# Kernel optimization log

Hardware: AMD Instinct MI355X
Metric: run time of the kernel (lower is better)

The kernel has to match this reference:

```python
import jax, jax.numpy as jnp
import numpy as np

B, T, C = 2, 2048, 1024
H = 16
D = C // H  # head_size = 64
FF = 4 * C
EPS = 1e-5


def _layernorm(x, g, b):
    mu = jnp.mean(x, axis=-1, keepdims=True)
    var = jnp.var(x, axis=-1, keepdims=True)
    return (x - mu) * jax.lax.rsqrt(var + EPS) * g + b


def setup_inputs() -> dict:
    key = jax.random.key(0)
    ks = jax.random.split(key, 12)
    s_in = 1.0 / np.sqrt(C)
    s_ff = 1.0 / np.sqrt(FF)
    return {
        "x": jax.random.normal(ks[0], (B, T, C), jnp.float32),
        "Wq": jax.random.uniform(ks[1], (H, C, D), jnp.float32, -s_in, s_in),
        "Wk": jax.random.uniform(ks[2], (H, C, D), jnp.float32, -s_in, s_in),
        "Wv": jax.random.uniform(ks[3], (H, C, D), jnp.float32, -s_in, s_in),
        "Wo": jax.random.uniform(ks[4], (C, C), jnp.float32, -s_in, s_in),
        "bo": jax.random.uniform(ks[5], (C,), jnp.float32, -s_in, s_in),
        "W1": jax.random.uniform(ks[6], (C, FF), jnp.float32, -s_in, s_in),
        "b1": jax.random.uniform(ks[7], (FF,), jnp.float32, -s_in, s_in),
        "W2": jax.random.uniform(ks[8], (FF, C), jnp.float32, -s_ff, s_ff),
        "b2": jax.random.uniform(ks[9], (C,), jnp.float32, -s_ff, s_ff),
        "g1": jnp.ones((C,), jnp.float32),
        "be1": jnp.zeros((C,), jnp.float32),
        "g2": jnp.ones((C,), jnp.float32),
        "be2": jnp.zeros((C,), jnp.float32),
    }


def reference(x, Wq, Wk, Wv, Wo, bo, W1, b1, W2, b2, g1, be1, g2, be2):
    h = _layernorm(x, g1, be1)
    # per-head projections (no bias), vectorized over heads
    q = jnp.einsum("btc,hcd->bhtd", h, Wq)
    k = jnp.einsum("btc,hcd->bhtd", h, Wk)
    v = jnp.einsum("btc,hcd->bhtd", h, Wv)
    # NOTE: original scales by n_embd**-0.5 (C, not head_size) -- faithful
    scores = jnp.einsum("bhtd,bhsd->bhts", q, k) * (C ** -0.5)
    causal = jnp.tril(jnp.ones((T, T), bool))
    scores = jnp.where(causal, scores, -jnp.inf)
    att = jax.nn.softmax(scores, axis=-1)
    out = jnp.einsum("bhts,bhsd->bhtd", att, v)
    out = out.transpose(0, 2, 1, 3).reshape(B, T, C)  # concat heads
    x = out @ Wo + bo + x  # attn residual (dropout=0 -> identity)
    h2 = _layernorm(x, g2, be2)
    ff = jax.nn.relu(h2 @ W1 + b1) @ W2 + b2
    return x + ff
```

## Files before the change

kernel.cpp:

```cpp
#include <hip/hip_runtime.h>
#include <stdint.h>

typedef unsigned short ushort_t;
typedef __attribute__((ext_vector_type(8))) short bf16x8;
typedef __attribute__((ext_vector_type(4))) float f32x4;

__device__ __forceinline__ unsigned short f2b(float f) {
  unsigned u = __float_as_uint(f);
  u += 0x7fffu + ((u >> 16) & 1u);
  return (unsigned short)(u >> 16);
}

__device__ __forceinline__ void async16(const void* g, void* l) {
  __builtin_amdgcn_global_load_lds(
      (const __attribute__((address_space(1))) void*)g,
      (__attribute__((address_space(3))) void*)l, 16, 0, 0);
}

__global__ __launch_bounds__(256) void ln_kernel(
    const float* __restrict__ x, const float* __restrict__ g,
    const float* __restrict__ be, ushort_t* __restrict__ out) {
  const int C = 1024;
  int row = blockIdx.x;
  const float4* xr = (const float4*)(x + (size_t)row * C);
  int tid = threadIdx.x;
  float4 v = xr[tid];
  float s = v.x + v.y + v.z + v.w;
  float sq = v.x * v.x + v.y * v.y + v.z * v.z + v.w * v.w;
  #pragma unroll
  for (int off = 32; off > 0; off >>= 1) {
    s += __shfl_xor(s, off);
    sq += __shfl_xor(sq, off);
  }
  __shared__ float ss[4], ssq[4];
  int wv = tid >> 6;
  if ((tid & 63) == 0) { ss[wv] = s; ssq[wv] = sq; }
  __syncthreads();
  s = ss[0] + ss[1] + ss[2] + ss[3];
  sq = ssq[0] + ssq[1] + ssq[2] + ssq[3];
  float mu = s * (1.f / C);
  float var = sq * (1.f / C) - mu * mu;
  float rs = rsqrtf(var + 1e-5f);
  float4 gv = ((const float4*)g)[tid];
  float4 bv = ((const float4*)be)[tid];
  ushort4 o;
  o.x = f2b((v.x - mu) * rs * gv.x + bv.x);
  o.y = f2b((v.y - mu) * rs * gv.y + bv.y);
  o.z = f2b((v.z - mu) * rs * gv.z + bv.z);
  o.w = f2b((v.w - mu) * rs * gv.w + bv.w);
  ((ushort4*)(out + (size_t)row * C))[tid] = o;
}

__global__ __launch_bounds__(256) void reduce2_kernel(
    const float* __restrict__ p0, const float* __restrict__ p1,
    const float* __restrict__ bias, const float* __restrict__ resid,
    float* __restrict__ out) {
  int idx = blockIdx.x * 256 + threadIdx.x;
  float4 a = ((const float4*)p0)[idx];
  float4 b = ((const float4*)p1)[idx];
  float4 r = ((const float4*)resid)[idx];
  float4 bi = ((const float4*)bias)[idx & 255];
  float4 o;
  o.x = a.x + b.x + r.x + bi.x;
  o.y = a.y + b.y + r.y + bi.y;
  o.z = a.z + b.z + r.z + bi.z;
  o.w = a.w + b.w + r.w + bi.w;
  ((float4*)out)[idx] = o;
}

__global__ __launch_bounds__(256) void transpose_all_kernel(
    const float* __restrict__ Wq, const float* __restrict__ Wk,
    const float* __restrict__ Wv, const float* __restrict__ Wo,
    const float* __restrict__ W1, const float* __restrict__ W2,
    ushort_t* __restrict__ qkvt, ushort_t* __restrict__ wot,
    ushort_t* __restrict__ w1t, ushort_t* __restrict__ w2t) {
  int bid = blockIdx.x;
  const float* in;
  ushort_t* out;
  int R, Cin, bx, by;
  if (bid < 3072) {
    int z = bid >> 6, rem = bid & 63;
    bx = rem & 1; by = rem >> 1;
    int wsel = z >> 4, h = z & 15;
    in = (wsel == 0 ? Wq : wsel == 1 ? Wk : Wv) + (size_t)h * 1024 * 64;
    out = qkvt + (size_t)wsel * 1024 * 1024 + (size_t)h * 1024 * 64;
    R = 1024; Cin = 64;
  } else if (bid < 4096) {
    int rem = bid - 3072;
    bx = rem & 31; by = rem >> 5;
    in = Wo; out = wot; R = 1024; Cin = 1024;
  } else if (bid < 8192) {
    int rem = bid - 4096;
    bx = rem & 127; by = rem >> 7;
    in = W1; out = w1t; R = 1024; Cin = 4096;
  } else {
    int rem = bid - 8192;
    bx = rem & 31; by = rem >> 5;
    in = W2; out = w2t; R = 4096; Cin = 1024;
  }
  __shared__ float tile[32][33];
  int c0 = bx * 32, r0 = by * 32;
  int tx = threadIdx.x, ty = threadIdx.y;
  #pragma unroll
  for (int i = 0; i < 4; i++)
    tile[ty + 8 * i][tx] = in[(size_t)(r0 + ty + 8 * i) * Cin + c0 + tx];
  __syncthreads();
  #pragma unroll
  for (int i = 0; i < 4; i++)
    out[(size_t)(c0 + ty + 8 * i) * R + r0 + tx] = f2b(tile[tx][ty + 8 * i]);
}

__global__ __launch_bounds__(256) void transpose_v_kernel(
    const ushort_t* __restrict__ qkv, ushort_t* __restrict__ vt) {
  __shared__ ushort_t tile[32][33];
  int bh = blockIdx.z;
  int b = bh >> 4, h = bh & 15;
  int d0 = blockIdx.x * 32, t0 = blockIdx.y * 32;
  int tx = threadIdx.x, ty = threadIdx.y;
  #pragma unroll
  for (int i = 0; i < 4; i++)
    tile[ty + 8 * i][tx] =
        qkv[(size_t)(b * 2048 + t0 + ty + 8 * i) * 3072 + 2048 + h * 64 + d0 + tx];
  __syncthreads();
  #pragma unroll
  for (int i = 0; i < 4; i++)
    vt[(size_t)(bh * 64 + d0 + ty + 8 * i) * 2048 + t0 + tx] = tile[tx][ty + 8 * i];
}

template <int BN, int N, int K, int FLAGS, int SK>
__global__ __launch_bounds__(256, 3) void gemm_bt_kernel(
    const ushort_t* __restrict__ A, const ushort_t* __restrict__ Bt,
    const float* __restrict__ bias, const float* __restrict__ resid,
    void* __restrict__ outv, float* __restrict__ pp0, float* __restrict__ pp1) {
  constexpr int KS = K / SK;
  __shared__ ushort_t Als[2][128 * 32];
  __shared__ ushort_t Bls[2][128 * 32];
  int tid = threadIdx.x, w = tid >> 6, lane = tid & 63, quad = lane >> 4, l16 = lane & 15;
  int fid = blockIdx.x;
  int bn_low = (fid >> 3) & 7;
  int meta = (fid & 7) | ((fid >> 6) << 3);
  int bm = meta & 31;
  int high = meta >> 5;
  int bn, zz;
  if constexpr (SK > 1) { zz = high; bn = bn_low; }
  else { zz = 0; bn = bn_low + 8 * high; }
  int bn0 = bn * 128, bm0 = bm * 128;
  int koff = (SK > 1) ? zz * KS : 0;
  int wm = (w >> 1) * 64, wn = (w & 1) * 64;
  f32x4 acc[4][4];
  #pragma unroll
  for (int i = 0; i < 4; i++)
    #pragma unroll
    for (int j = 0; j < 4; j++) acc[i][j] = f32x4{0.f, 0.f, 0.f, 0.f};
  const ushort_t* Ag = A + (size_t)bm0 * K + koff;
  const ushort_t* Bg = Bt + (size_t)bn0 * K + koff;
  int lr = lane >> 2, lco = (lane & 3) * 8;
  auto stage = [&](int k0, int bi) {
    async16(Ag + (size_t)(w * 32 + lr) * K + k0 + lco, &Als[bi][w * 1024]);
    async16(Ag + (size_t)(w * 32 + 16 + lr) * K + k0 + lco, &Als[bi][w * 1024 + 512]);
    async16(Bg + (size_t)(w * 32 + lr) * K + k0 + lco, &Bls[bi][w * 1024]);
    async16(Bg + (size_t)(w * 32 + 16 + lr) * K + k0 + lco, &Bls[bi][w * 1024 + 512]);
  };
  stage(0, 0);
  int s = 0;
  for (int k0 = 0; k0 < KS; k0 += 32, s ^= 1) {
    __syncthreads();
    if (k0 + 32 < KS) stage(k0 + 32, s ^ 1);
    bf16x8 af[4], bf[4];
    #pragma unroll
    for (int i = 0; i < 4; i++)
      af[i] = *(const bf16x8*)&Als[s][(wm + i * 16 + l16) * 32 + quad * 8];
    #pragma unroll
    for (int j = 0; j < 4; j++)
      bf[j] = *(const bf16x8*)&Bls[s][(wn + j * 16 + l16) * 32 + quad * 8];
    #pragma unroll
    for (int i = 0; i < 4; i++)
      #pragma unroll
      for (int j = 0; j < 4; j++)
        acc[i][j] = __builtin_amdgcn_mfma_f32_16x16x32_bf16(af[i], bf[j], acc[i][j], 0, 0, 0);
  }
  float* pdst = nullptr;
  if constexpr (SK > 1) pdst = zz ? pp1 : pp0;
  #pragma unroll
  for (int i = 0; i < 4; i++)
    #pragma unroll
    for (int j = 0; j < 4; j++)
      #pragma unroll
      for (int r = 0; r < 4; r++) {
        int row = bm0 + wm + i * 16 + quad * 4 + r;
        int col = bn0 + wn + j * 16 + l16;
        float v = acc[i][j][r];
        if constexpr (SK > 1) {
          pdst[(size_t)row * N + col] = v;
        } else {
          if constexpr (FLAGS & 4) v += bias[col];
          if constexpr (FLAGS & 8) v += resid[(size_t)row * N + col];
          if constexpr (FLAGS & 1) v = fmaxf(v, 0.f);
          if constexpr ((FLAGS & 2) != 0)
            ((ushort_t*)outv)[(size_t)row * N + col] = f2b(v);
          else
            ((float*)outv)[(size_t)row * N + col] = v;
        }
      }
}

template <int N, int K, int FLAGS, int SK>
__global__ __launch_bounds__(256, 3) void gemm_bt64_kernel(
    const ushort_t* __restrict__ A, const ushort_t* __restrict__ Bt,
    const float* __restrict__ bias, const float* __restrict__ resid,
    void* __restrict__ outv, float* __restrict__ pp0, float* __restrict__ pp1) {
  constexpr int KS = K / SK;
  constexpr int NBM = 32;
  constexpr int NBN = N / 64;
  constexpr int NWG = NBM * NBN * SK;
  __shared__ ushort_t Als[2][128 * 32];
  __shared__ ushort_t Bls[2][64 * 32];
  int tid = threadIdx.x, w = tid >> 6, lane = tid & 63, quad = lane >> 4, l16 = lane & 15;
  int bid = blockIdx.x;
  int swz = (bid & 7) * (NWG / 8) + (bid >> 3);
  int z = 0;
  if constexpr (SK > 1) { z = swz / (NBM * NBN); swz -= z * (NBM * NBN); }
  int bm = swz / NBN, bn = swz - bm * NBN;
  int bm0 = bm * 128, bn0 = bn * 64;
  int koff = z * KS;
  int wm = (w >> 1) * 64, wn = (w & 1) * 32;
  f32x4 acc[4][2];
  #pragma unroll
  for (int i = 0; i < 4; i++)
    #pragma unroll
    for (int j = 0; j < 2; j++) acc[i][j] = f32x4{0.f, 0.f, 0.f, 0.f};
  const ushort_t* Ag = A + (size_t)bm0 * K + koff;
  const ushort_t* Bg = Bt + (size_t)bn0 * K + koff;
  int lr = lane >> 2, lco = (lane & 3) * 8;
  auto stage = [&](int k0, int bi) {
    async16(Ag + (size_t)(w * 32 + lr) * K + k0 + lco, &Als[bi][w * 1024]);
    async16(Ag + (size_t)(w * 32 + 16 + lr) * K + k0 + lco, &Als[bi][w * 1024 + 512]);
    async16(Bg + (size_t)(w * 16 + lr) * K + k0 + lco, &Bls[bi][w * 512]);
  };
  stage(0, 0);
  int s = 0;
  for (int k0 = 0; k0 < KS; k0 += 32, s ^= 1) {
    __syncthreads();
    if (k0 + 32 < KS) stage(k0 + 32, s ^ 1);
    bf16x8 af[4], bf[2];
    #pragma unroll
    for (int i = 0; i < 4; i++)
      af[i] = *(const bf16x8*)&Als[s][(wm + i * 16 + l16) * 32 + quad * 8];
    #pragma unroll
    for (int j = 0; j < 2; j++)
      bf[j] = *(const bf16x8*)&Bls[s][(wn + j * 16 + l16) * 32 + quad * 8];
    #pragma unroll
    for (int i = 0; i < 4; i++)
      #pragma unroll
      for (int j = 0; j < 2; j++)
        acc[i][j] = __builtin_amdgcn_mfma_f32_16x16x32_bf16(af[i], bf[j], acc[i][j], 0, 0, 0);
  }
  float* pdst = nullptr;
  if constexpr (SK > 1) pdst = z ? pp1 : pp0;
  #pragma unroll
  for (int i = 0; i < 4; i++)
    #pragma unroll
    for (int j = 0; j < 2; j++)
      #pragma unroll
      for (int r = 0; r < 4; r++) {
        int row = bm0 + wm + i * 16 + quad * 4 + r;
        int col = bn0 + wn + j * 16 + l16;
        float v = acc[i][j][r];
        if constexpr (SK > 1) {
          pdst[(size_t)row * N + col] = v;
        } else {
          if constexpr (FLAGS & 4) v += bias[col];
          if constexpr (FLAGS & 8) v += resid[(size_t)row * N + col];
          if constexpr (FLAGS & 1) v = fmaxf(v, 0.f);
          if constexpr ((FLAGS & 2) != 0)
            ((ushort_t*)outv)[(size_t)row * N + col] = f2b(v);
          else
            ((float*)outv)[(size_t)row * N + col] = v;
        }
      }
}

__global__ __launch_bounds__(256, 4) void attn_kernel(
    const ushort_t* __restrict__ qkv, const ushort_t* __restrict__ vt,
    ushort_t* __restrict__ out) {
  const int T = 2048, CC = 3072;
  __shared__ ushort_t Kls[2][2 * 64 * 32];
  __shared__ ushort_t Vls[2][2 * 64 * 32];
  int fid = blockIdx.x;
  int bh = (fid & 7) * 4 + ((fid >> 3) & 3);
  int qb = 31 - (fid >> 5);
  int b = bh >> 4, h = bh & 15;
  int q0 = qb * 64;
  int tid = threadIdx.x, w = tid >> 6, lane = tid & 63, quad = lane >> 4, l16 = lane & 15;
  int srow = w * 16 + (lane >> 2);
  int sco = (lane & 3) * 8;
  const ushort_t* kg = qkv + (size_t)(b * T + srow) * CC + 1024 + h * 64 + sco;
  const ushort_t* vg = vt + (size_t)(bh * 64 + srow) * T + sco;
  int q0s = q0 + w * 16;
  int trow = q0s + l16;
  const ushort_t* qp = qkv + (size_t)(b * T + trow) * CC + h * 64 + quad * 8;
  bf16x8 aq[2] = { *(const bf16x8*)qp, *(const bf16x8*)(qp + 32) };
  f32x4 O[4];
  #pragma unroll
  for (int i = 0; i < 4; i++) O[i] = f32x4{0.f, 0.f, 0.f, 0.f};
  float mrun = -1e30f, lrun = 0.f;
  const float ksc = 0.03125f * 1.44269504f;
  int src0 = (quad & 1) * 32 + l16;
  int src1 = src0 + 16;
  bool hiq = quad >= 2;
  auto stage = [&](int kb, int bi) {
    int s0 = kb * 64;
    async16(kg + (size_t)s0 * CC, &Kls[bi][w * 512]);
    async16(kg + (size_t)s0 * CC + 32, &Kls[bi][2048 + w * 512]);
    async16(vg + s0, &Vls[bi][w * 512]);
    async16(vg + s0 + 32, &Vls[bi][2048 + w * 512]);
  };
  stage(0, 0);
  for (int kb = 0; kb <= qb; kb++) {
    __syncthreads();
    if (kb < qb) stage(kb + 1, (kb + 1) & 1);
    int bi = kb & 1;
    int s0 = kb * 64;
    bf16x8 kfr[4][2], vfr[4][2];
    #pragma unroll
    for (int t = 0; t < 4; t++)
      #pragma unroll
      for (int ks = 0; ks < 2; ks++) {
        kfr[t][ks] = *(const bf16x8*)&Kls[bi][(ks * 64 + t * 16 + l16) * 32 + quad * 8];
        vfr[t][ks] = *(const bf16x8*)&Vls[bi][(ks * 64 + t * 16 + l16) * 32 + quad * 8];
      }
    f32x4 st[4];
    #pragma unroll
    for (int t = 0; t < 4; t++) {
      st[t] = f32x4{0.f, 0.f, 0.f, 0.f};
      #pragma unroll
      for (int ks = 0; ks < 2; ks++)
        st[t] = __builtin_amdgcn_mfma_f32_16x16x32_bf16(kfr[t][ks], aq[ks], st[t], 0, 0, 0);
    }
    float sv[4][4];
    float vmax = -1e30f;
    if (kb == qb) {
      #pragma unroll
      for (int t = 0; t < 4; t++)
        #pragma unroll
        for (int r = 0; r < 4; r++) {
          float sc = st[t][r] * ksc;
          int scol = s0 + t * 16 + quad * 4 + r;
          if (scol > trow) sc = -1e30f;
          sv[t][r] = sc;
          vmax = fmaxf(vmax, sc);
        }
    } else {
      #pragma unroll
      for (int t = 0; t < 4; t++)
        #pragma unroll
        for (int r = 0; r < 4; r++) {
          float sc = st[t][r] * ksc;
          sv[t][r] = sc;
          vmax = fmaxf(vmax, sc);
        }
    }
    vmax = fmaxf(vmax, __shfl_xor(vmax, 16));
    vmax = fmaxf(vmax, __shfl_xor(vmax, 32));
    float mnew = fmaxf(mrun, vmax);
    float alpha = __builtin_amdgcn_exp2f(mrun - mnew);
    mrun = mnew;
    float psum = 0.f;
    int pk[4][2];
    #pragma unroll
    for (int t = 0; t < 4; t++) {
      float p0 = __builtin_amdgcn_exp2f(sv[t][0] - mnew);
      float p1 = __builtin_amdgcn_exp2f(sv[t][1] - mnew);
      float p2 = __builtin_amdgcn_exp2f(sv[t][2] - mnew);
      float p3 = __builtin_amdgcn_exp2f(sv[t][3] - mnew);
      psum += (p0 + p1) + (p2 + p3);
      pk[t][0] = (int)((unsigned)f2b(p0) | ((unsigned)f2b(p1) << 16));
      pk[t][1] = (int)((unsigned)f2b(p2) | ((unsigned)f2b(p3) << 16));
    }
    psum += __shfl_xor(psum, 16);
    psum += __shfl_xor(psum, 32);
    lrun = lrun * alpha + psum;
    #pragma unroll
    for (int dt = 0; dt < 4; dt++) O[dt] *= alpha;
    #pragma unroll
    for (int g32 = 0; g32 < 2; g32++) {
      int t0 = 2 * g32, t1 = t0 + 1;
      int a0 = __shfl(pk[t0][0], src0), b0 = __shfl(pk[t1][0], src0);
      int a1 = __shfl(pk[t0][1], src0), b1 = __shfl(pk[t1][1], src0);
      int a2 = __shfl(pk[t0][0], src1), b2 = __shfl(pk[t1][0], src1);
      int a3 = __shfl(pk[t0][1], src1), b3 = __shfl(pk[t1][1], src1);
      union { int4 i; bf16x8 h; } u;
      u.i.x = hiq ? b0 : a0;
      u.i.y = hiq ? b1 : a1;
      u.i.z = hiq ? b2 : a2;
      u.i.w = hiq ? b3 : a3;
      #pragma unroll
      for (int dt = 0; dt < 4; dt++)
        O[dt] = __builtin_amdgcn_mfma_f32_16x16x32_bf16(vfr[dt][g32], u.h, O[dt], 0, 0, 0);
    }
  }
  float inv = 1.f / lrun;
  #pragma unroll
  for (int dt = 0; dt < 4; dt++) {
    ushort4 o;
    unsigned short* op = (unsigned short*)&o;
    #pragma unroll
    for (int r = 0; r < 4; r++) op[r] = f2b(O[dt][r] * inv);
    *(ushort4*)&out[(size_t)(b * T + trow) * 1024 + h * 64 + dt * 16 + quad * 4] = o;
  }
}

extern "C" void kernel_launch(void* const* d_in, const int* in_sizes, int n_in,
                              void* d_out, int out_size, void* d_ws, size_t ws_size,
                              hipStream_t stream) {
  const int B = 2, T = 2048, C = 1024, H = 16, D = 64, FF = 4096;
  const int M = B * T;
  const float* x   = (const float*)d_in[0];
  const float* Wq  = (const float*)d_in[1];
  const float* Wk  = (const float*)d_in[2];
  const float* Wv  = (const float*)d_in[3];
  const float* Wo  = (const float*)d_in[4];
  const float* bo  = (const float*)d_in[5];
  const float* W1  = (const float*)d_in[6];
  const float* b1  = (const float*)d_in[7];
  const float* W2  = (const float*)d_in[8];
  const float* b2  = (const float*)d_in[9];
  const float* g1  = (const float*)d_in[10];
  const float* be1 = (const float*)d_in[11];
  const float* g2  = (const float*)d_in[12];
  const float* be2 = (const float*)d_in[13];
  float* out = (float*)d_out;

  char* ws = (char*)d_ws;
  size_t off = 0;
  auto alloc = [&](size_t bytes) {
    void* p = ws + off;
    off += (bytes + 255) & ~(size_t)255;
    return p;
  };
  ushort_t* qkvt = (ushort_t*)alloc((size_t)3 * C * C * 2);
  ushort_t* wot  = (ushort_t*)alloc((size_t)C * C * 2);
  ushort_t* w1t  = (ushort_t*)alloc((size_t)FF * C * 2);
  ushort_t* w2t  = (ushort_t*)alloc((size_t)C * FF * 2);
  ushort_t* hbuf = (ushort_t*)alloc((size_t)M * C * 2);
  ushort_t* big  = (ushort_t*)alloc((size_t)M * FF * 2);
  ushort_t* vtb  = (ushort_t*)alloc((size_t)M * C * 2);
  ushort_t* aout = (ushort_t*)alloc((size_t)M * C * 2);
  float*    x2   = (float*)alloc((size_t)M * C * 4);
  float* pf0 = (float*)vtb;
  float* pf1 = (float*)qkvt;

  dim3 tb(32, 8);
  transpose_all_kernel<<<12288, tb, 0, stream>>>(
      Wq, Wk, Wv, Wo, W1, W2, qkvt, wot, w1t, w2t);
  ln_kernel<<<M, 256, 0, stream>>>(x, g1, be1, hbuf);
  gemm_bt_kernel<24, 3072, 1024, 2, 1><<<768, 256, 0, stream>>>(
      hbuf, qkvt, nullptr, nullptr, big, nullptr, nullptr);
  transpose_v_kernel<<<dim3(2, T / 32, B * H), tb, 0, stream>>>(big, vtb);
  attn_kernel<<<1024, 256, 0, stream>>>(big, vtb, aout);
  gemm_bt64_kernel<1024, 1024, 4 | 8, 1><<<512, 256, 0, stream>>>(
      aout, wot, bo, x, x2, nullptr, nullptr);
  ln_kernel<<<M, 256, 0, stream>>>(x2, g2, be2, hbuf);
  gemm_bt_kernel<32, 4096, 1024, 1 | 2 | 4, 1><<<1024, 256, 0, stream>>>(
      hbuf, w1t, b1, nullptr, big, nullptr, nullptr);
  gemm_bt64_kernel<1024, 4096, 0, 2><<<1024, 256, 0, stream>>>(
      big, w2t, nullptr, nullptr, nullptr, pf0, pf1);
  reduce2_kernel<<<M * C / 1024, 256, 0, stream>>>(pf0, pf1, b2, x2, out);
}
```

Before: 360.4 us.

## Replace 128x128 GEMM with 256x256 8-wave ping-pong pipelined kernel for QKV and FFN1

Swaps the 128x128 tile, 4-wave GEMM used for the QKV projection and the first FFN layer for a 256x256 tile, 8-wave kernel. It uses a K-step of 64, XOR-swizzled LDS layout, double buffering with interleaved async loads, explicit barriers, and setprio around the MFMA phases. The goal is more data reuse per loaded tile, fewer LDS bank conflicts and better overlap of loads with MFMA work. The cost is far fewer workgroups (192 and 256) on a GPU with many CUs, which risks poor occupancy and wave-quantisation idle time, plus high register pressure from the 8x4 accumulators.

```diff
diff --git a/kernel.cpp b/kernel.cpp
--- a/kernel.cpp
+++ b/kernel.cpp
@@ -127,82 +127,146 @@
     vt[(size_t)(bh * 64 + d0 + ty + 8 * i) * 2048 + t0 + tx] = tile[tx][ty + 8 * i];
 }
 
-template <int BN, int N, int K, int FLAGS, int SK>
-__global__ __launch_bounds__(256, 3) void gemm_bt_kernel(
+#define RD_A(DB, MB) \
+  _Pragma("unroll") \
+  for (int mf_ = 0; mf_ < 4; mf_++) { \
+    af[(MB) + mf_][0] = *(const bf16x8*)&Als[DB][wm][(aRow + ((MB) + mf_) * 16) * 64 + rof0]; \
+    af[(MB) + mf_][1] = *(const bf16x8*)&Als[DB][wm][(aRow + ((MB) + mf_) * 16) * 64 + rof1]; \
+  }
+#define RD_B(DB, NB) \
+  _Pragma("unroll") \
+  for (int nf_ = 0; nf_ < 2; nf_++) { \
+    bf[(NB) + nf_][0] = *(const bf16x8*)&Bls[DB][bh][(bRow + ((NB) + nf_) * 16) * 64 + rof0]; \
+    bf[(NB) + nf_][1] = *(const bf16x8*)&Bls[DB][bh][(bRow + ((NB) + nf_) * 16) * 64 + rof1]; \
+  }
+#define MMPH(MB, NB) \
+  __builtin_amdgcn_s_barrier(); \
+  asm volatile("s_waitcnt lgkmcnt(0)" ::: "memory"); \
+  __builtin_amdgcn_sched_barrier(0); \
+  __builtin_amdgcn_s_setprio(1); \
+  _Pragma("unroll") \
+  for (int mf_ = 0; mf_ < 4; mf_++) \
+    _Pragma("unroll") \
+    for (int nf_ = 0; nf_ < 2; nf_++) { \
+      acc[(MB) + mf_][(NB) + nf_] = __builtin_amdgcn_mfma_f32_16x16x32_bf16( \
+          af[(MB) + mf_][0], bf[(NB) + nf_][0], acc[(MB) + mf_][(NB) + nf_], 0, 0, 0); \
+      acc[(MB) + mf_][(NB) + nf_] = __builtin_amdgcn_mfma_f32_16x16x32_bf16( \
+          af[(MB) + mf_][1], bf[(NB) + nf_][1], acc[(MB) + mf_][(NB) + nf_], 0, 0, 0); \
+    } \
+  __builtin_amdgcn_s_setprio(0);
+#define ENDPH __builtin_amdgcn_s_barrier();
+
+template <int N, int K, int FLAGS>
+__global__ __launch_bounds__(512, 2) void gemm256p8_kernel(
     const ushort_t* __restrict__ A, const ushort_t* __restrict__ Bt,
-    const float* __restrict__ bias, const float* __restrict__ resid,
-    void* __restrict__ outv, float* __restrict__ pp0, float* __restrict__ pp1) {
-  constexpr int KS = K / SK;
-  __shared__ ushort_t Als[2][128 * 32];
-  __shared__ ushort_t Bls[2][128 * 32];
-  int tid = threadIdx.x, w = tid >> 6, lane = tid & 63, quad = lane >> 4, l16 = lane & 15;
-  int fid = blockIdx.x;
-  int bn_low = (fid >> 3) & 7;
-  int meta = (fid & 7) | ((fid >> 6) << 3);
-  int bm = meta & 31;
-  int high = meta >> 5;
-  int bn, zz;
-  if constexpr (SK > 1) { zz = high; bn = bn_low; }
-  else { zz = 0; bn = bn_low + 8 * high; }
-  int bn0 = bn * 128, bm0 = bm * 128;
-  int koff = (SK > 1) ? zz * KS : 0;
-  int wm = (w >> 1) * 64, wn = (w & 1) * 64;
-  f32x4 acc[4][4];
-  #pragma unroll
-  for (int i = 0; i < 4; i++)
-    #pragma unroll
-    for (int j = 0; j < 4; j++) acc[i][j] = f32x4{0.f, 0.f, 0.f, 0.f};
-  const ushort_t* Ag = A + (size_t)bm0 * K + koff;
-  const ushort_t* Bg = Bt + (size_t)bn0 * K + koff;
-  int lr = lane >> 2, lco = (lane & 3) * 8;
-  auto stage = [&](int k0, int bi) {
-    async16(Ag + (size_t)(w * 32 + lr) * K + k0 + lco, &Als[bi][w * 1024]);
-    async16(Ag + (size_t)(w * 32 + 16 + lr) * K + k0 + lco, &Als[bi][w * 1024 + 512]);
-    async16(Bg + (size_t)(w * 32 + lr) * K + k0 + lco, &Bls[bi][w * 1024]);
-    async16(Bg + (size_t)(w * 32 + 16 + lr) * K + k0 + lco, &Bls[bi][w * 1024 + 512]);
+    const float* __restrict__ bias, void* __restrict__ outv) {
+  constexpr int NBN = N / 256;
+  constexpr int NT2 = K / 128;
+  __shared__ __align__(16) ushort_t Als[2][2][128 * 64];
+  __shared__ __align__(16) ushort_t Bls[2][2][128 * 64];
+  int tid = threadIdx.x, w = tid >> 6, lane = tid & 63;
+  int quad = lane >> 4, l16 = lane & 15;
+  int wm = w >> 2, wn = w & 3;
+  int bid = blockIdx.x;
+  int bm = bid / NBN, bn = bid % NBN;
+  int bm0 = bm * 256, bn0 = bn * 256;
+  int lrow = (w << 3) + (lane >> 3);
+  int kc8 = ((lane & 7) ^ ((lane >> 3) & 7)) << 3;
+  const ushort_t* Ab = A + (size_t)(bm0 + lrow) * K + kc8;
+  const ushort_t* Bb = Bt + (size_t)(bn0 + lrow) * K + kc8;
+  int rof0 = (quad ^ (l16 & 7)) << 3;
+  int rof1 = ((4 + quad) ^ (l16 & 7)) << 3;
+  int bh = wn >> 1;
+  int aRow = l16;
+  int bRow = (wn & 1) * 64 + l16;
+
+  auto stA = [&](int kt, int half, int db) {
+    const ushort_t* g = Ab + (size_t)(half * 128) * K + kt * 64;
+    ushort_t* l = &Als[db][half][w * 512];
+    async16(g, l);
+    async16(g + (size_t)64 * K, l + 4096);
   };
-  stage(0, 0);
-  int s = 0;
-  for (int k0 = 0; k0 < KS; k0 += 32, s ^= 1) {
-    __syncthreads();
-    if (k0 + 32 < KS) stage(k0 + 32, s ^ 1);
-    bf16x8 af[4], bf[4];
-    #pragma unroll
-    for (int i = 0; i < 4; i++)
-      af[i] = *(const bf16x8*)&Als[s][(wm + i * 16 + l16) * 32 + quad * 8];
-    #pragma unroll
-    for (int j = 0; j < 4; j++)
-      bf[j] = *(const bf16x8*)&Bls[s][(wn + j * 16 + l16) * 32 + quad * 8];
-    #pragma unroll
-    for (int i = 0; i < 4; i++)
-      #pragma unroll
-      for (int j = 0; j < 4; j++)
-        acc[i][j] = __builtin_amdgcn_mfma_f32_16x16x32_bf16(af[i], bf[j], acc[i][j], 0, 0, 0);
-  }
-  float* pdst = nullptr;
-  if constexpr (SK > 1) pdst = zz ? pp1 : pp0;
-  #pragma unroll
-  for (int i = 0; i < 4; i++)
-    #pragma unroll
-    for (int j = 0; j < 4; j++)
+  auto stB = [&](int kt, int half, int db) {
+    const ushort_t* g = Bb + (size_t)(half * 128) * K + kt * 64;
+    ushort_t* l = &Bls[db][half][w * 512];
+    async16(g, l);
+    async16(g + (size_t)64 * K, l + 4096);
+  };
+
+  f32x4 acc[8][4];
+  #pragma unroll
+  for (int mf = 0; mf < 8; mf++)
+    #pragma unroll
+    for (int nf = 0; nf < 4; nf++) acc[mf][nf] = f32x4{0.f, 0.f, 0.f, 0.f};
+  bf16x8 af[8][2], bf[4][2];
+
+  stA(0, 0, 0); stA(0, 1, 0);
+  stB(0, 0, 0); stB(0, 1, 0);
+  stA(1, 0, 1); stA(1, 1, 1);
+  asm volatile("s_waitcnt vmcnt(4)" ::: "memory");
+  __builtin_amdgcn_s_barrier();
+
+  #pragma unroll 1
+  for (int i = 0; i < NT2; ++i) {
+    bool lastI = (i == NT2 - 1);
+    int t1 = 2 * i + 1;
+    RD_A(0, 0)
+    RD_B(0, 0)
+    stB(t1, 0, 1);
+    MMPH(0, 0)
+    ENDPH
+    RD_A(0, 4)
+    stB(t1, 1, 1);
+    MMPH(4, 0)
+    ENDPH
+    RD_B(0, 2)
+    if (!lastI) stA(t1 + 1, 0, 0);
+    MMPH(4, 2)
+    ENDPH
+    if (!lastI) stA(t1 + 1, 1, 0);
+    MMPH(0, 2)
+    if (!lastI) asm volatile("s_waitcnt vmcnt(4)" ::: "memory");
+    else        asm volatile("s_waitcnt vmcnt(0)" ::: "memory");
+    ENDPH
+    RD_A(1, 0)
+    RD_B(1, 0)
+    if (!lastI) stB(t1 + 1, 0, 0);
+    MMPH(0, 0)
+    ENDPH
+    RD_A(1, 4)
+    if (!lastI) stB(t1 + 1, 1, 0);
+    MMPH(4, 0)
+    ENDPH
+    RD_B(1, 2)
+    if (!lastI) stA(t1 + 2, 0, 1);
+    MMPH(4, 2)
+    ENDPH
+    if (!lastI) stA(t1 + 2, 1, 1);
+    MMPH(0, 2)
+    if (!lastI) asm volatile("s_waitcnt vmcnt(4)" ::: "memory");
+    ENDPH
+  }
+  #pragma unroll
+  for (int mf = 0; mf < 8; mf++)
+    #pragma unroll
+    for (int nf = 0; nf < 4; nf++)
       #pragma unroll
       for (int r = 0; r < 4; r++) {
-        int row = bm0 + wm + i * 16 + quad * 4 + r;
-        int col = bn0 + wn + j * 16 + l16;
-        float v = acc[i][j][r];
-        if constexpr (SK > 1) {
-          pdst[(size_t)row * N + col] = v;
-        } else {
-          if constexpr (FLAGS & 4) v += bias[col];
-          if constexpr (FLAGS & 8) v += resid[(size_t)row * N + col];
-          if constexpr (FLAGS & 1) v = fmaxf(v, 0.f);
-          if constexpr ((FLAGS & 2) != 0)
-            ((ushort_t*)outv)[(size_t)row * N + col] = f2b(v);
-          else
-            ((float*)outv)[(size_t)row * N + col] = v;
-        }
+        int row = bm0 + wm * 128 + mf * 16 + quad * 4 + r;
+        int col = bn0 + wn * 64 + nf * 16 + l16;
+        float v = acc[mf][nf][r];
+        if constexpr (FLAGS & 4) v += bias[col];
+        if constexpr (FLAGS & 1) v = fmaxf(v, 0.f);
+        if constexpr ((FLAGS & 2) != 0)
+          ((ushort_t*)outv)[(size_t)row * N + col] = f2b(v);
+        else
+          ((float*)outv)[(size_t)row * N + col] = v;
       }
 }
+#undef RD_A
+#undef RD_B
+#undef MMPH
+#undef ENDPH
 
 template <int N, int K, int FLAGS, int SK>
 __global__ __launch_bounds__(256, 3) void gemm_bt64_kernel(
@@ -454,15 +518,15 @@
   transpose_all_kernel<<<12288, tb, 0, stream>>>(
       Wq, Wk, Wv, Wo, W1, W2, qkvt, wot, w1t, w2t);
   ln_kernel<<<M, 256, 0, stream>>>(x, g1, be1, hbuf);
-  gemm_bt_kernel<24, 3072, 1024, 2, 1><<<768, 256, 0, stream>>>(
-      hbuf, qkvt, nullptr, nullptr, big, nullptr, nullptr);
+  gemm256p8_kernel<3072, 1024, 2><<<192, 512, 0, stream>>>(
+      hbuf, qkvt, nullptr, big);
   transpose_v_kernel<<<dim3(2, T / 32, B * H), tb, 0, stream>>>(big, vtb);
   attn_kernel<<<1024, 256, 0, stream>>>(big, vtb, aout);
   gemm_bt64_kernel<1024, 1024, 4 | 8, 1><<<512, 256, 0, stream>>>(
       aout, wot, bo, x, x2, nullptr, nullptr);
   ln_kernel<<<M, 256, 0, stream>>>(x2, g2, be2, hbuf);
-  gemm_bt_kernel<32, 4096, 1024, 1 | 2 | 4, 1><<<1024, 256, 0, stream>>>(
-      hbuf, w1t, b1, nullptr, big, nullptr, nullptr);
+  gemm256p8_kernel<4096, 1024, 1 | 2 | 4><<<256, 512, 0, stream>>>(
+      hbuf, w1t, b1, big);
   gemm_bt64_kernel<1024, 4096, 0, 2><<<1024, 256, 0, stream>>>(
       big, w2t, nullptr, nullptr, nullptr, pf0, pf1);
   reduce2_kernel<<<M * C / 1024, 256, 0, stream>>>(pf0, pf1, b2, x2, out);
```

Result: no change. 355.7 us (-1.3%).
